# Performance work log

Hardware: AMD Instinct MI355X
Metric: run time of the kernel (lower is better)

The kernel has to match this reference:

```python
import jax, jax.numpy as jnp
import numpy as np

EPS = 1e-5

def _layernorm(x, g, b):
    mu = jnp.mean(x, axis=-1, keepdims=True)
    var = jnp.var(x, axis=-1, keepdims=True)
    return (x - mu) * jax.lax.rsqrt(var + EPS) * g + b

def _attn(x, Wq, bq, Wk, bk, Wv, bv):
    # torch Linear: y = x @ W.T + b, W is [out, in]
    q = jnp.einsum('bse,oe->bso', x, Wq) + bq
    k = jnp.einsum('bse,oe->bso', x, Wk) + bk
    v = jnp.einsum('bse,oe->bso', x, Wv) + bv
    S = x.shape[1]
    # NOTE: original scales by sqrt(seq_len) (the 'C' dim), reproduced faithfully
    att = jnp.einsum('bqd,bkd->bqk', q, k) / jnp.sqrt(jnp.asarray(S, x.dtype))
    att = jax.nn.softmax(att, axis=-1)
    return jnp.einsum('bqk,bkd->bqd', att, v)

def setup_inputs() -> dict:
    key = jax.random.key(0)
    ks = jax.random.split(key, 16)
    B, S, E = 4, 4096, 256
    sc = 1.0 / np.sqrt(E)
    d = {'x': jax.random.normal(ks[0], (B, S, E), jnp.float32)}
    names = ['Wq1', 'Wk1', 'Wv1', 'Wq2', 'Wk2', 'Wv2']
    for i, n in enumerate(names):
        d[n] = jax.random.normal(ks[1 + i], (E, E), jnp.float32) * sc
        d['b' + n[1:]] = jnp.zeros((E,), jnp.float32)
    d['g1'] = jnp.ones((E,), jnp.float32)
    d['beta1'] = jnp.zeros((E,), jnp.float32)
    d['g2'] = jnp.ones((E,), jnp.float32)
    d['beta2'] = jnp.zeros((E,), jnp.float32)
    return d

def reference(x, Wq1, bq1, Wk1, bk1, Wv1, bv1, Wq2, bq2, Wk2, bk2, Wv2, bv2, g1, beta1, g2, beta2):
    o = _layernorm(_attn(x, Wq1, bq1, Wk1, bk1, Wv1, bv1) + x, g1, beta1)
    f = _attn(o, Wq2, bq2, Wk2, bk2, Wv2, bv2)
    return _layernorm(f + o, g2, beta2)
```

## Files before the change

### kernel.cpp

```cpp
#include <hip/hip_runtime.h>
#include <hip/hip_bf16.h>


typedef __attribute__((ext_vector_type(8))) short bf16x8;
typedef __attribute__((ext_vector_type(4))) float f32x4;
typedef __attribute__((ext_vector_type(16))) float f32x16;
typedef __attribute__((ext_vector_type(4))) int i32x4;
typedef __attribute__((ext_vector_type(8))) int i32x8;
typedef unsigned char u8;

#define MFMA_BF16(A, B, C) __builtin_amdgcn_mfma_f32_16x16x32_bf16(A, B, C, 0, 0, 0)
#define MFMA_SC(A, B, C, SA, SB)                                                \
    __builtin_amdgcn_mfma_scale_f32_32x32x64_f8f6f4(A, B, C, 0, 0, 0, SA, 0, SB)
#define SCALE_1  0x7F7F7F7Fu
#define SCALE_Q  0x79797979u

#define CP16(g, l)                                                              \
    __builtin_amdgcn_global_load_lds(                                           \
        (const __attribute__((address_space(1))) void*)(g),                     \
        (__attribute__((address_space(3))) void*)(l), 16, 0, 0)

static __device__ __forceinline__ float fexp2(float x) {
    float r;
    asm("v_exp_f32 %0, %1" : "=v"(r) : "v"(x));
    return r;
}

static __device__ __forceinline__ short f2bf(float f) {
    __hip_bfloat16 h = __float2bfloat16(f);
    return __builtin_bit_cast(short, h);
}
static __device__ __forceinline__ float bf2f(short s) {
    unsigned int u = ((unsigned int)(unsigned short)s) << 16;
    return __builtin_bit_cast(float, u);
}
static __device__ __forceinline__ float ld1(const float* p) { return *p; }
static __device__ __forceinline__ float ld1(const short* p) { return bf2f(*p); }
static __device__ __forceinline__ void st1(float* p, float v) { *p = v; }
static __device__ __forceinline__ void st1(short* p, float v) { *p = f2bf(v); }

static __device__ __forceinline__ u8 f2fp8(float f) {
    return (u8)(__builtin_amdgcn_cvt_pk_fp8_f32(f, f, 0, false) & 0xff);
}
static __device__ __forceinline__ unsigned int pk4fp8(float a, float b, float c, float d) {
    int w = __builtin_amdgcn_cvt_pk_fp8_f32(a, b, 0, false);
    w = __builtin_amdgcn_cvt_pk_fp8_f32(c, d, w, true);
    return (unsigned int)w;
}

static __device__ __forceinline__ bf16x8 ldA8(const short* p) {
    return *reinterpret_cast<const bf16x8*>(p);
}
static __device__ __forceinline__ bf16x8 ldA8(const float* p) {
    float4 f0 = *reinterpret_cast<const float4*>(p);
    float4 f1 = *reinterpret_cast<const float4*>(p + 4);
    bf16x8 r;
    r[0] = f2bf(f0.x); r[1] = f2bf(f0.y); r[2] = f2bf(f0.z); r[3] = f2bf(f0.w);
    r[4] = f2bf(f1.x); r[5] = f2bf(f1.y); r[6] = f2bf(f1.z); r[7] = f2bf(f1.w);
    return r;
}

static __device__ __forceinline__ i32x8 cat(i32x4 lo, i32x4 hi) {
    i32x8 r;
    r[0] = lo[0]; r[1] = lo[1]; r[2] = lo[2]; r[3] = lo[3];
    r[4] = hi[0]; r[5] = hi[1]; r[6] = hi[2]; r[7] = hi[3];
    return r;
}

template <int NCH256>
static __device__ __forceinline__ void stage_rows(const short* __restrict__ g,
                                                  short* s, int tid) {
    const int wave = tid >> 6;
#pragma unroll
    for (int j = 0; j < NCH256; ++j) {
        const int idx = j * 256 + tid;
        const int row = idx >> 5, c = idx & 31;
        CP16(g + row * 256 + ((c ^ (row & 7)) << 3),
             s + ((j * 256 + wave * 64) << 3));
    }
}
static __device__ __forceinline__ void stage_k(const u8* __restrict__ g,
                                               u8* s, int tid) {
    const int wave = tid >> 6;
#pragma unroll
    for (int j = 0; j < 4; ++j) {
        const int idx = j * 256 + tid;
        CP16(g + (idx << 4), s + ((j * 256 + wave * 64) << 4));
    }
}
static __device__ __forceinline__ void stage_v(const u8* __restrict__ g,
                                               u8* s, int tid) {
    const int wave = tid >> 6;
#pragma unroll
    for (int j = 0; j < 4; ++j) {
        const int idx = j * 256 + tid;
        CP16(g + ((idx >> 2) * 4096) + ((idx & 3) << 4),
             s + ((j * 256 + wave * 64) << 4));
    }
}

__global__ __launch_bounds__(256) void cvt_w_kernel(
    const float* __restrict__ w0, const float* __restrict__ w1,
    const float* __restrict__ w2, const float* __restrict__ w3,
    const float* __restrict__ w4, const float* __restrict__ w5,
    short* __restrict__ wb)
{
    const int idx = (blockIdx.x * 256 + threadIdx.x) * 8;
    const int w = idx >> 16, off = idx & 65535;
    const float* src = w0;
    if (w == 1) src = w1;
    else if (w == 2) src = w2;
    else if (w == 3) src = w3;
    else if (w == 4) src = w4;
    else if (w == 5) src = w5;
    *reinterpret_cast<bf16x8*>(wb + w * 65536 + off) = ldA8(src + off);
}

template <typename TX>
__global__ __launch_bounds__(256, 2) void qkv_proj_kernel(
    const TX* __restrict__ X, const short* __restrict__ Wb,
    const float* __restrict__ bq, const float* __restrict__ bk,
    const float* __restrict__ bv,
    u8* __restrict__ Qo, u8* __restrict__ Ko, u8* __restrict__ VTo)
{
    __shared__ __attribute__((aligned(16))) short Wt[128 * 256];
    const int tid  = threadIdx.x;
    const int lane = tid & 63;
    const int wave = tid >> 6;
    const int c16  = lane & 15;
    const int quad = lane >> 4;
    const int which = blockIdx.y;
    const int m0 = blockIdx.x * 64 + wave * 16;

    const short* W    = Wb + which * 65536;
    const float* bias = (which == 0) ? bq : (which == 1) ? bk : bv;

    bf16x8 a[8];
#pragma unroll
    for (int ke = 0; ke < 8; ++ke)
        a[ke] = ldA8(X + (m0 + c16) * 256 + ke * 32 + quad * 8);

    f32x4 acc[16];
#pragma unroll
    for (int nb = 0; nb < 16; ++nb) { f32x4 z = {0.f, 0.f, 0.f, 0.f}; acc[nb] = z; }

#pragma unroll
    for (int half = 0; half < 2; ++half) {
        if (half) __syncthreads();
        stage_rows<16>(W + half * 128 * 256, Wt, tid);
        __syncthreads();
#pragma unroll
        for (int nb8 = 0; nb8 < 8; ++nb8) {
            const int nb = half * 8 + nb8;
            const short* wr = Wt + (nb8 * 16 + c16) * 256;
#pragma unroll
            for (int ke = 0; ke < 8; ++ke) {
                bf16x8 b = *reinterpret_cast<const bf16x8*>(
                    wr + (((ke * 4 + quad) ^ (c16 & 7)) << 3));
                acc[nb] = MFMA_BF16(a[ke], b, acc[nb]);
            }
        }
    }

    if (which == 0) {
        constexpr float L2E = 1.4426950408889634f;
#pragma unroll
        for (int nb = 0; nb < 16; ++nb) {
            const int o = nb * 16 + c16;
            const float bb_ = bias[o];
#pragma unroll
            for (int r = 0; r < 4; ++r)
                Qo[(m0 + quad * 4 + r) * 256 + o] = f2fp8((acc[nb][r] + bb_) * L2E);
        }
    } else if (which == 1) {
#pragma unroll
        for (int nb = 0; nb < 16; ++nb) {
            const int o = nb * 16 + c16;
            const float bb_ = bias[o];
#pragma unroll
            for (int r = 0; r < 4; ++r) {
                const int row = m0 + quad * 4 + r;
                Ko[row * 256 + (((nb ^ (row & 15)) << 4) | c16)] =
                    f2fp8(acc[nb][r] + bb_);
            }
        }
    } else {
#pragma unroll
        for (int nb = 0; nb < 16; ++nb) {
            const int o = nb * 16 + c16;
            const float bb_ = bias[o];
            const int row = m0 + quad * 4;
            const int batch = row >> 12;
            const int n = row & 4095;
            const int nsw = (n & ~63) | ((((n >> 4) ^ (o >> 1)) & 3) << 4) |
                            (n & 12);
            unsigned int pk = pk4fp8(acc[nb][0] + bb_, acc[nb][1] + bb_,
                                     acc[nb][2] + bb_, acc[nb][3] + bb_);
            *reinterpret_cast<unsigned int*>(
                VTo + (size_t)batch * (256 * 4096) + o * 4096 + nsw) = pk;
        }
    }
}

__global__ __launch_bounds__(256, 2) void attn_part_kernel(
    const u8* __restrict__ Qb, const u8* __restrict__ Kb,
    const u8* __restrict__ VTb,
    short* __restrict__ Op, float* __restrict__ Lo)
{
    __shared__ __attribute__((aligned(16))) u8 Kt[2][64 * 256];
    __shared__ __attribute__((aligned(16))) u8 Vt[2][256 * 64];

    const int tid  = threadIdx.x;
    const int lane = tid & 63;
    const int wave = tid >> 6;
    const int l31  = lane & 31;
    const int hi   = lane >> 5;
    const int c16  = lane & 15;
    const int bi = blockIdx.x;
    const int combo = ((bi & 7) << 1) | (bi >> 8);
    const int batch = combo >> 2;
    const int ks    = combo & 3;
    const int qt    = (bi >> 3) & 31;
    const size_t bb = (size_t)batch * (4096 * 256);
    const int rw = qt * 128 + wave * 32;
    const int kbase = ks * 1024;

    i32x8 qf[4];
#pragma unroll
    for (int ke = 0; ke < 4; ++ke) {
        const u8* qp = Qb + bb + (rw + l31) * 256 + ke * 64 + hi * 32;
        qf[ke] = cat(*reinterpret_cast<const i32x4*>(qp),
                     *reinterpret_cast<const i32x4*>(qp + 16));
    }

    f32x16 z16;
#pragma unroll
    for (int i = 0; i < 16; ++i) z16[i] = 0.f;
    f32x16 oa[8];
#pragma unroll
    for (int et = 0; et < 8; ++et) oa[et] = z16;
    f32x16 lacc = z16;

    i32x8 onesf;
#pragma unroll
    for (int i = 0; i < 8; ++i) onesf[i] = 0x38383838;

    int kx0[4], kx1[4];
#pragma unroll
    for (int ke = 0; ke < 4; ++ke) {
        kx0[ke] = ((ke * 4 + hi * 2) ^ c16) << 4;
        kx1[ke] = ((ke * 4 + hi * 2 + 1) ^ c16) << 4;
    }
    const int vsw = (l31 >> 1) & 3;
    const int vx0 = ((hi * 2) ^ vsw) << 4;
    const int vx1 = ((hi * 2 + 1) ^ vsw) << 4;

    const u8* Kg = Kb + bb + kbase * 256;
    const u8* Vg = VTb + bb + kbase;

    f32x16 s0, s1;
    auto compute_st = [&](const u8* K) {
        const u8* kp = K + l31 * 256;
        s0 = z16; s1 = z16;
        __builtin_amdgcn_s_setprio(1);
#pragma unroll
        for (int ke = 0; ke < 4; ++ke) {
            i32x8 a0 = cat(*reinterpret_cast<const i32x4*>(kp + kx0[ke]),
                           *reinterpret_cast<const i32x4*>(kp + kx1[ke]));
            s0 = MFMA_SC(a0, qf[ke], s0, SCALE_1, SCALE_Q);
            i32x8 a1 = cat(*reinterpret_cast<const i32x4*>(kp + 8192 + kx0[ke]),
                           *reinterpret_cast<const i32x4*>(kp + 8192 + kx1[ke]));
            s1 = MFMA_SC(a1, qf[ke], s1, SCALE_1, SCALE_Q);
        }
        __builtin_amdgcn_s_setprio(0);
    };

    stage_k(Kg, &Kt[0][0], tid);
    stage_v(Vg, &Vt[0][0], tid);
    __syncthreads();
    compute_st(&Kt[0][0]);
    stage_k(Kg + 64 * 256, &Kt[1][0], tid);
    stage_v(Vg + 64, &Vt[1][0], tid);

    for (int kt = 0; kt < 16; ++kt) {
        unsigned int dw0[4], dw1[4];
#pragma unroll
        for (int g = 0; g < 4; ++g) {
            const float p00 = fexp2(s0[4 * g + 0]);
            const float p01 = fexp2(s0[4 * g + 1]);
            const float p02 = fexp2(s0[4 * g + 2]);
            const float p03 = fexp2(s0[4 * g + 3]);
            const float p10 = fexp2(s1[4 * g + 0]);
            const float p11 = fexp2(s1[4 * g + 1]);
            const float p12 = fexp2(s1[4 * g + 2]);
            const float p13 = fexp2(s1[4 * g + 3]);
            dw0[g] = pk4fp8(p00, p01, p02, p03);
            dw1[g] = pk4fp8(p10, p11, p12, p13);
        }
#pragma unroll
        for (int g = 0; g < 4; ++g)
            asm volatile("v_permlane32_swap_b32 %0, %1"
                         : "+v"(dw0[g]), "+v"(dw1[g]));
        i32x8 pf;
        pf[0] = (int)dw0[0]; pf[1] = (int)dw1[0];
        pf[2] = (int)dw0[1]; pf[3] = (int)dw1[1];
        pf[4] = (int)dw0[2]; pf[5] = (int)dw1[2];
        pf[6] = (int)dw0[3]; pf[7] = (int)dw1[3];

        {
            const u8* V = &Vt[kt & 1][0];
            __builtin_amdgcn_s_setprio(1);
#pragma unroll
            for (int et = 0; et < 8; ++et) {
                const u8* vp = V + (et * 32 + l31) * 64;
                i32x8 b = cat(*reinterpret_cast<const i32x4*>(vp + vx0),
                              *reinterpret_cast<const i32x4*>(vp + vx1));
                oa[et] = MFMA_SC(pf, b, oa[et], SCALE_1, SCALE_1);
            }
            lacc = MFMA_SC(pf, onesf, lacc, SCALE_1, SCALE_1);
            __builtin_amdgcn_s_setprio(0);
        }

        if (kt < 15) {
            __syncthreads();
            if (kt < 14) {
                stage_k(Kg + (kt + 2) * 64 * 256, &Kt[kt & 1][0], tid);
                stage_v(Vg + (kt + 2) * 64, &Vt[kt & 1][0], tid);
            }
            compute_st(&Kt[(kt + 1) & 1][0]);
        }
    }

    const size_t base = (size_t)ks * 16384 + batch * 4096 + rw;
#pragma unroll
    for (int et = 0; et < 8; ++et)
#pragma unroll
        for (int r = 0; r < 16; ++r) {
            const int qr = (r & 3) + 8 * (r >> 2) + 4 * hi;
            Op[(base + qr) * 256 + et * 32 + l31] = f2bf(oa[et][r]);
        }
    if (l31 == 0) {
#pragma unroll
        for (int r = 0; r < 16; ++r) {
            const int qr = (r & 3) + 8 * (r >> 2) + 4 * hi;
            Lo[base + qr] = lacc[r];
        }
    }
}

template <typename TRES, typename TOUT>
__global__ __launch_bounds__(256) void merge_ln_kernel(
    const short* __restrict__ Op, const float* __restrict__ Lo,
    const TRES* __restrict__ res, const float* __restrict__ gamma,
    const float* __restrict__ beta, TOUT* __restrict__ out)
{
    const int lane = threadIdx.x & 63;
    const int wave = threadIdx.x >> 6;
    const int row = blockIdx.x * 4 + wave;
    const float li = 1.0f / (Lo[row] + Lo[16384 + row] +
                             Lo[32768 + row] + Lo[49152 + row]);
    const int e = lane * 4;
    float o[4] = {0.f, 0.f, 0.f, 0.f};
#pragma unroll
    for (int s = 0; s < 4; ++s) {
        ushort4 u = *reinterpret_cast<const ushort4*>(
            Op + ((size_t)s * 16384 + row) * 256 + e);
        o[0] += bf2f((short)u.x);
        o[1] += bf2f((short)u.y);
        o[2] += bf2f((short)u.z);
        o[3] += bf2f((short)u.w);
    }
    float y[4];
#pragma unroll
    for (int i = 0; i < 4; ++i)
        y[i] = o[i] * li + ld1(res + (size_t)row * 256 + e + i);

    float sum = y[0] + y[1] + y[2] + y[3];
    float sq  = y[0]*y[0] + y[1]*y[1] + y[2]*y[2] + y[3]*y[3];
#pragma unroll
    for (int d = 1; d < 64; d <<= 1) {
        sum += __shfl_xor(sum, d, 64);
        sq  += __shfl_xor(sq,  d, 64);
    }
    const float mean = sum * (1.0f / 256.0f);
    const float var  = sq * (1.0f / 256.0f) - mean * mean;
    const float rstd = rsqrtf(var + 1e-5f);
#pragma unroll
    for (int i = 0; i < 4; ++i)
        st1(out + (size_t)row * 256 + e + i,
            (y[i] - mean) * rstd * gamma[e + i] + beta[e + i]);
}

extern "C" void kernel_launch(void* const* d_in, const int* in_sizes, int n_in,
                              void* d_out, int out_size, void* d_ws, size_t ws_size,
                              hipStream_t stream) {
    const float* x   = (const float*)d_in[0];
    const float* Wq1 = (const float*)d_in[1];
    const float* bq1 = (const float*)d_in[2];
    const float* Wk1 = (const float*)d_in[3];
    const float* bk1 = (const float*)d_in[4];
    const float* Wv1 = (const float*)d_in[5];
    const float* bv1 = (const float*)d_in[6];
    const float* Wq2 = (const float*)d_in[7];
    const float* bq2 = (const float*)d_in[8];
    const float* Wk2 = (const float*)d_in[9];
    const float* bk2 = (const float*)d_in[10];
    const float* Wv2 = (const float*)d_in[11];
    const float* bv2 = (const float*)d_in[12];
    const float* g1  = (const float*)d_in[13];
    const float* be1 = (const float*)d_in[14];
    const float* g2  = (const float*)d_in[15];
    const float* be2 = (const float*)d_in[16];

    const size_t NE = (size_t)16384 * 256;
    short* O1  = (short*)d_ws;
    short* Wb  = O1 + NE;
    u8*    Qb  = (u8*)(Wb + 6 * 65536);
    u8*    Kb  = Qb + NE;
    u8*    VTb = Kb + NE;
    short* Op  = (short*)(VTb + NE);
    float* Lo  = (float*)(Op + 4 * NE);
    float* outp = (float*)d_out;

    dim3 pgrid(256, 3), pblk(256);

    cvt_w_kernel<<<192, 256, 0, stream>>>(Wq1, Wk1, Wv1, Wq2, Wk2, Wv2, Wb);

    qkv_proj_kernel<float><<<pgrid, pblk, 0, stream>>>(
        x, Wb, bq1, bk1, bv1, Qb, Kb, VTb);
    attn_part_kernel<<<512, 256, 0, stream>>>(Qb, Kb, VTb, Op, Lo);
    merge_ln_kernel<float, short><<<4096, 256, 0, stream>>>(Op, Lo, x, g1, be1, O1);

    qkv_proj_kernel<short><<<pgrid, pblk, 0, stream>>>(
        O1, Wb + 3 * 65536, bq2, bk2, bv2, Qb, Kb, VTb);
    attn_part_kernel<<<512, 256, 0, stream>>>(Qb, Kb, VTb, Op, Lo);
    merge_ln_kernel<short, float><<<4096, 256, 0, stream>>>(Op, Lo, O1, g2, be2, outp);
}
```

Before: 226.9 us.

## Read V operand directly from global memory instead of staging through LDS

Removes the LDS double buffer for the transposed V tile and has each lane load its V MFMA operand straight from global memory. The V projection writes a plain, unswizzled layout to match. This frees 32KB of LDS per block and removes the V staging copies, but every wave now fetches the same V data separately from global/L2, and those loads sit in the critical path without async prefetch.

```diff
diff --git a/kernel.cpp b/kernel.cpp
--- a/kernel.cpp
+++ b/kernel.cpp
@@ -86,16 +86,6 @@
     for (int j = 0; j < 4; ++j) {
         const int idx = j * 256 + tid;
         CP16(g + (idx << 4), s + ((j * 256 + wave * 64) << 4));
-    }
-}
-static __device__ __forceinline__ void stage_v(const u8* __restrict__ g,
-                                               u8* s, int tid) {
-    const int wave = tid >> 6;
-#pragma unroll
-    for (int j = 0; j < 4; ++j) {
-        const int idx = j * 256 + tid;
-        CP16(g + ((idx >> 2) * 4096) + ((idx & 3) << 4),
-             s + ((j * 256 + wave * 64) << 4));
     }
 }
 
@@ -192,12 +182,10 @@
             const int row = m0 + quad * 4;
             const int batch = row >> 12;
             const int n = row & 4095;
-            const int nsw = (n & ~63) | ((((n >> 4) ^ (o >> 1)) & 3) << 4) |
-                            (n & 12);
             unsigned int pk = pk4fp8(acc[nb][0] + bb_, acc[nb][1] + bb_,
                                      acc[nb][2] + bb_, acc[nb][3] + bb_);
             *reinterpret_cast<unsigned int*>(
-                VTo + (size_t)batch * (256 * 4096) + o * 4096 + nsw) = pk;
+                VTo + (size_t)batch * (256 * 4096) + o * 4096 + n) = pk;
         }
     }
 }
@@ -208,7 +196,6 @@
     short* __restrict__ Op, float* __restrict__ Lo)
 {
     __shared__ __attribute__((aligned(16))) u8 Kt[2][64 * 256];
-    __shared__ __attribute__((aligned(16))) u8 Vt[2][256 * 64];
 
     const int tid  = threadIdx.x;
     const int lane = tid & 63;
@@ -251,12 +238,9 @@
         kx0[ke] = ((ke * 4 + hi * 2) ^ c16) << 4;
         kx1[ke] = ((ke * 4 + hi * 2 + 1) ^ c16) << 4;
     }
-    const int vsw = (l31 >> 1) & 3;
-    const int vx0 = ((hi * 2) ^ vsw) << 4;
-    const int vx1 = ((hi * 2 + 1) ^ vsw) << 4;
 
     const u8* Kg = Kb + bb + kbase * 256;
-    const u8* Vg = VTb + bb + kbase;
+    const u8* Vg = VTb + bb + (size_t)l31 * 4096 + kbase;
 
     f32x16 s0, s1;
     auto compute_st = [&](const u8* K) {
@@ -276,11 +260,9 @@
     };
 
     stage_k(Kg, &Kt[0][0], tid);
-    stage_v(Vg, &Vt[0][0], tid);
     __syncthreads();
     compute_st(&Kt[0][0]);
     stage_k(Kg + 64 * 256, &Kt[1][0], tid);
-    stage_v(Vg + 64, &Vt[1][0], tid);
 
     for (int kt = 0; kt < 16; ++kt) {
         unsigned int dw0[4], dw1[4];
@@ -308,13 +290,13 @@
         pf[6] = (int)dw0[3]; pf[7] = (int)dw1[3];
 
         {
-            const u8* V = &Vt[kt & 1][0];
+            const u8* vk = Vg + kt * 64 + hi * 32;
             __builtin_amdgcn_s_setprio(1);
 #pragma unroll
             for (int et = 0; et < 8; ++et) {
-                const u8* vp = V + (et * 32 + l31) * 64;
-                i32x8 b = cat(*reinterpret_cast<const i32x4*>(vp + vx0),
-                              *reinterpret_cast<const i32x4*>(vp + vx1));
+                const u8* vp = vk + (size_t)et * (32 * 4096);
+                i32x8 b = cat(*reinterpret_cast<const i32x4*>(vp),
+                              *reinterpret_cast<const i32x4*>(vp + 16));
                 oa[et] = MFMA_SC(pf, b, oa[et], SCALE_1, SCALE_1);
             }
             lacc = MFMA_SC(pf, onesf, lacc, SCALE_1, SCALE_1);
@@ -323,10 +305,8 @@
 
         if (kt < 15) {
             __syncthreads();
-            if (kt < 14) {
+            if (kt < 14)
                 stage_k(Kg + (kt + 2) * 64 * 256, &Kt[kt & 1][0], tid);
-                stage_v(Vg + (kt + 2) * 64, &Vt[kt & 1][0], tid);
-            }
             compute_st(&Kt[(kt + 1) & 1][0]);
         }
     }
```

Measured after the change: 298.3 us. +31.5%, slower.

## Fuse Q/K/V projections per block with double-buffered weights; compute softmax sum in VALU

Applied to the files above, without the earlier changes.

The QKV projection kernel now has each block compute all three projections from one load of the X tile into registers. Weight halves are streamed through a double-buffered LDS staging area, so the next half loads while the current one is used. This removes the threefold re-read of X and the separate blockIdx.y launches, but leaves only 256 blocks, uses 128KB of LDS per block, and drops the 2-blocks-per-CU launch bound. In the attention kernel, the row sum of probabilities is now accumulated in fp32 on the VALU with a cross-half shuffle, instead of an extra MFMA against a ones matrix.

```diff
diff --git a/kernel.cpp b/kernel.cpp
--- a/kernel.cpp
+++ b/kernel.cpp
@@ -117,23 +117,19 @@
 }
 
 template <typename TX>
-__global__ __launch_bounds__(256, 2) void qkv_proj_kernel(
+__global__ __launch_bounds__(256) void qkv_proj_kernel(
     const TX* __restrict__ X, const short* __restrict__ Wb,
     const float* __restrict__ bq, const float* __restrict__ bk,
     const float* __restrict__ bv,
     u8* __restrict__ Qo, u8* __restrict__ Ko, u8* __restrict__ VTo)
 {
-    __shared__ __attribute__((aligned(16))) short Wt[128 * 256];
+    __shared__ __attribute__((aligned(16))) short Wt[2][128 * 256];
     const int tid  = threadIdx.x;
     const int lane = tid & 63;
     const int wave = tid >> 6;
     const int c16  = lane & 15;
     const int quad = lane >> 4;
-    const int which = blockIdx.y;
     const int m0 = blockIdx.x * 64 + wave * 16;
-
-    const short* W    = Wb + which * 65536;
-    const float* bias = (which == 0) ? bq : (which == 1) ? bk : bv;
 
     bf16x8 a[8];
 #pragma unroll
@@ -141,63 +137,76 @@
         a[ke] = ldA8(X + (m0 + c16) * 256 + ke * 32 + quad * 8);
 
     f32x4 acc[16];
-#pragma unroll
-    for (int nb = 0; nb < 16; ++nb) { f32x4 z = {0.f, 0.f, 0.f, 0.f}; acc[nb] = z; }
-
-#pragma unroll
-    for (int half = 0; half < 2; ++half) {
-        if (half) __syncthreads();
-        stage_rows<16>(W + half * 128 * 256, Wt, tid);
-        __syncthreads();
-#pragma unroll
-        for (int nb8 = 0; nb8 < 8; ++nb8) {
-            const int nb = half * 8 + nb8;
-            const short* wr = Wt + (nb8 * 16 + c16) * 256;
-#pragma unroll
-            for (int ke = 0; ke < 8; ++ke) {
-                bf16x8 b = *reinterpret_cast<const bf16x8*>(
-                    wr + (((ke * 4 + quad) ^ (c16 & 7)) << 3));
-                acc[nb] = MFMA_BF16(a[ke], b, acc[nb]);
-            }
-        }
-    }
-
-    if (which == 0) {
-        constexpr float L2E = 1.4426950408889634f;
-#pragma unroll
-        for (int nb = 0; nb < 16; ++nb) {
-            const int o = nb * 16 + c16;
-            const float bb_ = bias[o];
-#pragma unroll
-            for (int r = 0; r < 4; ++r)
-                Qo[(m0 + quad * 4 + r) * 256 + o] = f2fp8((acc[nb][r] + bb_) * L2E);
-        }
-    } else if (which == 1) {
-#pragma unroll
-        for (int nb = 0; nb < 16; ++nb) {
-            const int o = nb * 16 + c16;
-            const float bb_ = bias[o];
-#pragma unroll
-            for (int r = 0; r < 4; ++r) {
-                const int row = m0 + quad * 4 + r;
-                Ko[row * 256 + (((nb ^ (row & 15)) << 4) | c16)] =
-                    f2fp8(acc[nb][r] + bb_);
-            }
-        }
-    } else {
-#pragma unroll
-        for (int nb = 0; nb < 16; ++nb) {
-            const int o = nb * 16 + c16;
-            const float bb_ = bias[o];
-            const int row = m0 + quad * 4;
-            const int batch = row >> 12;
-            const int n = row & 4095;
-            const int nsw = (n & ~63) | ((((n >> 4) ^ (o >> 1)) & 3) << 4) |
-                            (n & 12);
-            unsigned int pk = pk4fp8(acc[nb][0] + bb_, acc[nb][1] + bb_,
-                                     acc[nb][2] + bb_, acc[nb][3] + bb_);
-            *reinterpret_cast<unsigned int*>(
-                VTo + (size_t)batch * (256 * 4096) + o * 4096 + nsw) = pk;
+
+    stage_rows<16>(Wb, &Wt[0][0], tid);
+
+#pragma unroll
+    for (int which = 0; which < 3; ++which) {
+        const float* bias = (which == 0) ? bq : (which == 1) ? bk : bv;
+#pragma unroll
+        for (int half = 0; half < 2; ++half) {
+            const int s = which * 2 + half;
+            __syncthreads();
+            if (s < 5)
+                stage_rows<16>(Wb + (s + 1) * 32768, &Wt[(s + 1) & 1][0], tid);
+            if (half == 0) {
+#pragma unroll
+                for (int nb = 0; nb < 16; ++nb) {
+                    f32x4 z = {0.f, 0.f, 0.f, 0.f};
+                    acc[nb] = z;
+                }
+            }
+#pragma unroll
+            for (int nb8 = 0; nb8 < 8; ++nb8) {
+                const int nb = half * 8 + nb8;
+                const short* wr = &Wt[s & 1][0] + (nb8 * 16 + c16) * 256;
+#pragma unroll
+                for (int ke = 0; ke < 8; ++ke) {
+                    bf16x8 b = *reinterpret_cast<const bf16x8*>(
+                        wr + (((ke * 4 + quad) ^ (c16 & 7)) << 3));
+                    acc[nb] = MFMA_BF16(a[ke], b, acc[nb]);
+                }
+            }
+        }
+
+        if (which == 0) {
+            constexpr float L2E = 1.4426950408889634f;
+#pragma unroll
+            for (int nb = 0; nb < 16; ++nb) {
+                const int o = nb * 16 + c16;
+                const float bb_ = bias[o];
+#pragma unroll
+                for (int r = 0; r < 4; ++r)
+                    Qo[(m0 + quad * 4 + r) * 256 + o] =
+                        f2fp8((acc[nb][r] + bb_) * L2E);
+            }
+        } else if (which == 1) {
+#pragma unroll
+            for (int nb = 0; nb < 16; ++nb) {
+                const int o = nb * 16 + c16;
+                const float bb_ = bias[o];
+#pragma unroll
+                for (int r = 0; r < 4; ++r) {
+                    const int row = m0 + quad * 4 + r;
+                    Ko[row * 256 + (((nb ^ (row & 15)) << 4) | c16)] =
+                        f2fp8(acc[nb][r] + bb_);
+                }
+            }
+        } else {
+#pragma unroll
+            for (int nb = 0; nb < 16; ++nb) {
+                const int o = nb * 16 + c16;
+                const float bb_ = bias[o];
+                const int row = m0 + quad * 4;
+                const int batch = row >> 12;
+                const int n = row & 4095;
+                const int nsw = (n & ~63) | ((((n >> 4) ^ (o >> 1)) & 3) << 4) |
+                                (n & 12);
+                unsigned int pk = pk4fp8(acc[nb][0] + bb_, acc[nb][1] + bb_,
+                                         acc[nb][2] + bb_, acc[nb][3] + bb_);
+                *reinterpret_cast<unsigned int*>(
+                    VTo + (size_t)batch * (256 * 4096) + o * 4096 + nsw) = pk;
+            }
         }
     }
 }
@@ -239,11 +248,7 @@
     f32x16 oa[8];
 #pragma unroll
     for (int et = 0; et < 8; ++et) oa[et] = z16;
-    f32x16 lacc = z16;
-
-    i32x8 onesf;
-#pragma unroll
-    for (int i = 0; i < 8; ++i) onesf[i] = 0x38383838;
+    float lsum = 0.f;
 
     int kx0[4], kx1[4];
 #pragma unroll
@@ -296,6 +301,7 @@
             const float p13 = fexp2(s1[4 * g + 3]);
             dw0[g] = pk4fp8(p00, p01, p02, p03);
             dw1[g] = pk4fp8(p10, p11, p12, p13);
+            lsum += ((p00 + p01) + (p02 + p03)) + ((p10 + p11) + (p12 + p13));
         }
 #pragma unroll
         for (int g = 0; g < 4; ++g)
@@ -317,7 +323,6 @@
                               *reinterpret_cast<const i32x4*>(vp + vx1));
                 oa[et] = MFMA_SC(pf, b, oa[et], SCALE_1, SCALE_1);
             }
-            lacc = MFMA_SC(pf, onesf, lacc, SCALE_1, SCALE_1);
             __builtin_amdgcn_s_setprio(0);
         }
 
@@ -331,6 +336,7 @@
         }
     }
 
+    const float rs = lsum + __shfl_xor(lsum, 32, 64);
     const size_t base = (size_t)ks * 16384 + batch * 4096 + rw;
 #pragma unroll
     for (int et = 0; et < 8; ++et)
@@ -339,13 +345,7 @@
             const int qr = (r & 3) + 8 * (r >> 2) + 4 * hi;
             Op[(base + qr) * 256 + et * 32 + l31] = f2bf(oa[et][r]);
         }
-    if (l31 == 0) {
-#pragma unroll
-        for (int r = 0; r < 16; ++r) {
-            const int qr = (r & 3) + 8 * (r >> 2) + 4 * hi;
-            Lo[base + qr] = lacc[r];
-        }
-    }
+    if (lane < 32) Lo[base + l31] = rs;
 }
 
 template <typename TRES, typename TOUT>
@@ -422,16 +422,14 @@
     float* Lo  = (float*)(Op + 4 * NE);
     float* outp = (float*)d_out;
 
-    dim3 pgrid(256, 3), pblk(256);
-
     cvt_w_kernel<<<192, 256, 0, stream>>>(Wq1, Wk1, Wv1, Wq2, Wk2, Wv2, Wb);
 
-    qkv_proj_kernel<float><<<pgrid, pblk, 0, stream>>>(
+    qkv_proj_kernel<float><<<256, 256, 0, stream>>>(
         x, Wb, bq1, bk1, bv1, Qb, Kb, VTb);
     attn_part_kernel<<<512, 256, 0, stream>>>(Qb, Kb, VTb, Op, Lo);
     merge_ln_kernel<float, short><<<4096, 256, 0, stream>>>(Op, Lo, x, g1, be1, O1);
 
-    qkv_proj_kernel<short><<<pgrid, pblk, 0, stream>>>(
+    qkv_proj_kernel<short><<<256, 256, 0, stream>>>(
         O1, Wb + 3 * 65536, bq2, bk2, bv2, Qb, Kb, VTb);
     attn_part_kernel<<<512, 256, 0, stream>>>(Qb, Kb, VTb, Op, Lo);
     merge_ln_kernel<short, float><<<4096, 256, 0, stream>>>(Op, Lo, O1, g2, be2, outp);
```

After: 230.5 us. Within noise of the previous version (+1.6%).
